# Performance work log

Hardware: AMD Instinct MI355X
Metric: run time of the kernel (lower is better)

Reference implementation:

```python
import jax, jax.numpy as jnp
import numpy as np
from jax import lax


def conv2d(x, w):
    # NCHW conv, stride 1, SAME padding, no bias (matches conv3x3/conv1x1 bias=False)
    return lax.conv_general_dilated(x, w, (1, 1), 'SAME',
                                    dimension_numbers=('NCHW', 'OIHW', 'NCHW'))


def scan_dir(x, w, b, axis, reverse):
    # IRNN recurrence along `axis`: h[t] = relu(w*h[t-1] + b + x[t]), h[0] = x[0]
    # w, b: per-channel scalars [C] (grouped 1x1 conv)
    xs = jnp.moveaxis(x, axis, 0)  # [T, B, C, L]
    if reverse:
        xs = xs[::-1]
    wb = w[None, :, None]
    bb = b[None, :, None]

    def step(h, xt):
        h = jax.nn.relu(wb * h + bb + xt)
        return h, h

    _, ys = lax.scan(step, xs[0], xs[1:])
    out = jnp.concatenate([xs[:1], ys], axis=0)
    if reverse:
        out = out[::-1]
    return jnp.moveaxis(out, 0, axis)


def irnn(x, ws, bs):
    # ws/bs: [4, C], direction order = up, right, down, left
    up = scan_dir(x, ws[0], bs[0], 2, True)
    right = scan_dir(x, ws[1], bs[1], 3, False)
    down = scan_dir(x, ws[2], bs[2], 2, False)
    left = scan_dir(x, ws[3], bs[3], 3, True)
    return jnp.concatenate([up, right, down, left], axis=1)  # [B, 4C, H, W]


def setup_inputs() -> dict:
    key = jax.random.key(0)
    ks = jax.random.split(key, 10)
    B, C, H, W = 8, 32, 256, 256
    x = jax.random.normal(ks[0], (B, C, H, W), jnp.float32)
    conv_in_w = jax.random.normal(ks[1], (C, C, 3, 3), jnp.float32) * 0.05
    conv2_w = jax.random.normal(ks[2], (C, 4 * C, 3, 3), jnp.float32) * 0.05
    conv3_w = jax.random.normal(ks[3], (C, 4 * C, 3, 3), jnp.float32) * 0.05
    conv_out_w = jax.random.normal(ks[4], (1, C, 1, 1), jnp.float32) * 0.05
    # grouped 1x1 conv weights: small magnitude keeps the 255-step recurrence stable
    irnn1_w = jax.random.uniform(ks[5], (4, C), jnp.float32, -0.2, 0.2)
    irnn1_b = jax.random.uniform(ks[6], (4, C), jnp.float32, -0.1, 0.1)
    irnn2_w = jax.random.uniform(ks[7], (4, C), jnp.float32, -0.2, 0.2)
    irnn2_b = jax.random.uniform(ks[8], (4, C), jnp.float32, -0.1, 0.1)
    return {"x": x, "conv_in_w": conv_in_w, "conv2_w": conv2_w,
            "conv3_w": conv3_w, "conv_out_w": conv_out_w,
            "irnn1_w": irnn1_w, "irnn1_b": irnn1_b,
            "irnn2_w": irnn2_w, "irnn2_b": irnn2_b}


def reference(x, conv_in_w, conv2_w, conv3_w, conv_out_w,
              irnn1_w, irnn1_b, irnn2_w, irnn2_b):
    # NOTE: torch's attention branch uses non-in-place .mul() whose result is
    # discarded, so attention has no effect on the output; omitted here.
    out = conv2d(x, conv_in_w)                                 # [B, C, H, W]
    out = conv2d(irnn(out, irnn1_w, irnn1_b), conv2_w)         # [B, C, H, W]
    out = jax.nn.relu(conv2d(irnn(out, irnn2_w, irnn2_b), conv3_w))
    mask = jax.nn.sigmoid(conv2d(out, conv_out_w))             # [B, 1, H, W]
    return mask
```

## Files before the change

kernel.cpp:

```cpp
#include <hip/hip_runtime.h>
#include <hip/hip_bf16.h>
#include <math.h>

static constexpr int Bn = 8, Cn = 32, Hn = 256, Wn = 256;
static constexpr int HP = 258;
static constexpr size_t PLANE = (size_t)Hn * Wn;

typedef __attribute__((ext_vector_type(8))) short bf16x8;
typedef __attribute__((ext_vector_type(4))) float f32x4;
typedef __attribute__((ext_vector_type(4))) short s16x4;
typedef __attribute__((ext_vector_type(4))) int   i32x4;

__device__ inline short bf16bits(float v) {
    union { __hip_bfloat16 h; short s; } u; u.h = __float2bfloat16(v);
    return u.s;
}
__device__ inline float bits2f(short s) {
    union { unsigned int u; float f; } u; u.u = ((unsigned int)(unsigned short)s) << 16;
    return u.f;
}
__device__ inline void async16(const short* g, short* l) {
    __builtin_amdgcn_global_load_lds(
        (const __attribute__((address_space(1))) unsigned int*)g,
        (__attribute__((address_space(3))) unsigned int*)l, 16, 0, 0);
}

template <int CIN>
__global__ __launch_bounds__(256) void pack_w(const float* __restrict__ w,
                                              __hip_bfloat16* __restrict__ wp)
{
    int idx = blockIdx.x * 256 + threadIdx.x;
    int j = idx & 7, g = (idx >> 3) & 3, m = (idx >> 5) & 15, mt = (idx >> 9) & 1;
    int rest = idx >> 10;
    int s = rest % 9, cb = rest / 9;
    int co = mt * 16 + m;
    int ci = cb * 32 + g * 8 + j;
    float v = w[((size_t)(co * CIN + ci) * 3 + s / 3) * 3 + (s % 3)];
    wp[idx] = __float2bfloat16(v);
}

template <int C>
__global__ __launch_bounds__(256) void zero_border(short* __restrict__ p)
{
    constexpr int CH8 = C / 8;
    int idx = blockIdx.x * 256 + threadIdx.x;
    if (idx >= 8 * 1028 * CH8) return;
    int c8 = idx % CH8;
    int rest = idx / CH8;
    int pe = rest % 1028, b = rest / 1028;
    int y, x;
    if (pe < 258)      { y = 0;   x = pe; }
    else if (pe < 516) { y = 257; x = pe - 258; }
    else if (pe < 772) { y = pe - 516 + 1; x = 0; }
    else               { y = pe - 772 + 1; x = 257; }
    *(i32x4*)(p + ((size_t)(b * HP + y) * HP + x) * C + c8 * 8) = i32x4{};
}

__global__ __launch_bounds__(256) void x_to_nhwc(const float* __restrict__ in,
                                                 __hip_bfloat16* __restrict__ out)
{
    __shared__ unsigned int shU[32 * 17];
    unsigned short* sh16 = (unsigned short*)shU;
    int tid = threadIdx.x;
    int px0 = blockIdx.x * 32;
    int b = blockIdx.y;
    const float2* in2 = (const float2*)(in + ((size_t)b * 32) * PLANE + px0);
    for (int i = tid; i < 512; i += 256) {
        int ch = i >> 4, pxp = i & 15;
        float2 v = in2[(size_t)ch * (PLANE / 2) + pxp];
        unsigned int lo = (unsigned short)bf16bits(v.x);
        unsigned int hi = (unsigned short)bf16bits(v.y);
        shU[ch * 17 + pxp] = lo | (hi << 16);
    }
    __syncthreads();
    int yy = px0 >> 8, xx0 = px0 & 255;
    unsigned int* out32 = (unsigned int*)out
        + ((size_t)(b * HP + yy + 1) * HP + xx0 + 1) * 16;
    for (int i = tid; i < 512; i += 256) {
        int px = i >> 4, chp = i & 15;
        unsigned int v = (unsigned int)sh16[(2 * chp) * 34 + px]
                       | ((unsigned int)sh16[(2 * chp + 1) * 34 + px] << 16);
        out32[(size_t)px * 16 + chp] = v;
    }
}

template <int CIN, bool RELU, bool FUSE>
__global__ __launch_bounds__(256, 2) void conv_mfma(const __hip_bfloat16* __restrict__ in,
        const __hip_bfloat16* __restrict__ wp, __hip_bfloat16* __restrict__ outA,
        const float* __restrict__ wo, float* __restrict__ outF)
{
    constexpr int CB = CIN / 32;
    constexpr int SLAB = 10880;
    constexpr int WSL  = 9216;
    constexpr int BUF  = SLAB + WSL;
    __shared__ short sIn[2 * BUF];
    int tid = threadIdx.x;
    int lane = tid & 63, wave = tid >> 6;
    int m = lane & 15, g = lane >> 4;
    int x0 = blockIdx.x * 32, y0 = blockIdx.y * 8, b = blockIdx.z;

    const short* inS = (const short*)in;
    const short* wpS = (const short*)wp;
    f32x4 acc[2][2][2] = {};

    auto stage = [&](int buf, int cb) {
        short* dst = sIn + buf * BUF;
        #pragma unroll
        for (int r = 0; r < 6; ++r) {
            int i = r * 256 + tid;
            if (r < 5 || i < 1360) {
                int ci16 = i & 3, q = i >> 2;
                int xx = q % 34, yy = q / 34;
                const short* gp = inS
                    + ((size_t)(b * HP + y0 + yy) * HP + x0 + xx) * CIN
                    + cb * 32 + ci16 * 8;
                async16(gp, dst + (r * 256 + wave * 64) * 8);
            }
        }
        #pragma unroll
        for (int r = 0; r < 5; ++r) {
            int i = r * 256 + tid;
            if (r < 4 || i < 1152) {
                const short* gp = wpS + (size_t)cb * WSL + i * 8;
                async16(gp, dst + SLAB * 1 + (r * 256 + wave * 64) * 8);
            }
        }
    };

    stage(0, 0);
    for (int cb = 0; cb < CB; ++cb) {
        __syncthreads();
        if (cb + 1 < CB) stage((cb + 1) & 1, cb + 1);
        const short* sb = sIn + (cb & 1) * BUF;
        const short* sw = sb + SLAB;

        #pragma unroll
        for (int s = 0; s < 9; ++s) {
            int dy = s / 3 - 1, dx = s % 3 - 1;
            bf16x8 wf0 = *(const bf16x8*)(sw + s * 1024 + (m * 4 + g) * 8);
            bf16x8 wf1 = *(const bf16x8*)(sw + s * 1024 + 512 + (m * 4 + g) * 8);
            #pragma unroll
            for (int wy = 0; wy < 2; ++wy) {
                int yy = wave * 2 + wy + dy + 1;
                const short* rp = sb + (yy * 34 + m + dx + 1) * 32 + g * 8;
                bf16x8 b0 = *(const bf16x8*)rp;
                bf16x8 b1 = *(const bf16x8*)(rp + 512);
                acc[wy][0][0] = __builtin_amdgcn_mfma_f32_16x16x32_bf16(wf0, b0, acc[wy][0][0], 0, 0, 0);
                acc[wy][1][0] = __builtin_amdgcn_mfma_f32_16x16x32_bf16(wf1, b0, acc[wy][1][0], 0, 0, 0);
                acc[wy][0][1] = __builtin_amdgcn_mfma_f32_16x16x32_bf16(wf0, b1, acc[wy][0][1], 0, 0, 0);
                acc[wy][1][1] = __builtin_amdgcn_mfma_f32_16x16x32_bf16(wf1, b1, acc[wy][1][1], 0, 0, 0);
            }
        }
    }

    if (FUSE) {
        float wv[2][4];
        #pragma unroll
        for (int mt = 0; mt < 2; ++mt)
            #pragma unroll
            for (int r = 0; r < 4; ++r) wv[mt][r] = wo[mt * 16 + g * 4 + r];
        #pragma unroll
        for (int wy = 0; wy < 2; ++wy) {
            int y = y0 + wave * 2 + wy;
            #pragma unroll
            for (int nt = 0; nt < 2; ++nt) {
                float s = 0.f;
                #pragma unroll
                for (int mt = 0; mt < 2; ++mt)
                    #pragma unroll
                    for (int r = 0; r < 4; ++r)
                        s = fmaf(fmaxf(acc[wy][mt][nt][r], 0.f), wv[mt][r], s);
                s += __shfl_xor(s, 16);
                s += __shfl_xor(s, 32);
                if (g == 0)
                    outF[(size_t)(b * 256 + y) * 256 + x0 + nt * 16 + m]
                        = 1.f / (1.f + expf(-s));
            }
        }
    } else {
        short* outS = (short*)outA;
        #pragma unroll
        for (int wy = 0; wy < 2; ++wy) {
            int y = y0 + wave * 2 + wy;
            #pragma unroll
            for (int nt = 0; nt < 2; ++nt) {
                int x = x0 + nt * 16 + m;
                size_t base = ((size_t)((b * 256 + y) * 256 + x)) * 32;
                #pragma unroll
                for (int mt = 0; mt < 2; ++mt) {
                    int co = mt * 16 + g * 4;
                    s16x4 ov;
                    #pragma unroll
                    for (int r = 0; r < 4; ++r) {
                        float v = acc[wy][mt][nt][r];
                        if (RELU) v = fmaxf(v, 0.f);
                        ov[r] = bf16bits(v);
                    }
                    *(s16x4*)(outS + base + co) = ov;
                }
            }
        }
    }
}

__global__ __launch_bounds__(256) void irnn_vert(const __hip_bfloat16* __restrict__ A,
        const float* __restrict__ w4, const float* __restrict__ b4,
        __hip_bfloat16* __restrict__ I)
{
    __shared__ short sA[64 * 256];
    int tid = threadIdx.x;
    int c = tid & 31, xo = tid >> 5;
    int x = blockIdx.x * 8 + xo;
    int y1 = blockIdx.y * 32;
    int b = blockIdx.z;
    const short* aS = (const short*)A;

    for (int i = tid; i < 2048; i += 256) {
        int slot = i >> 5, c8 = i & 31;
        int y = y1 - 16 + slot;
        if ((unsigned)y < (unsigned)Hn) {
            const short* gp = aS + ((size_t)(b * 256 + y) * 256 + blockIdx.x * 8) * 32 + c8 * 8;
            *(i32x4*)(sA + slot * 256 + c8 * 8) = *(const i32x4*)gp;
        }
    }
    __syncthreads();

    float wd = w4[2 * 32 + c], bd = b4[2 * 32 + c];
    float wu = w4[0 * 32 + c], bu = b4[0 * 32 + c];
    short* od = (short*)I + ((size_t)(b * HP + 1) * HP + 1 + x) * 128 + 2 * 32 + c;
    short* ou = (short*)I + ((size_t)(b * HP + 1) * HP + 1 + x) * 128 + 0 * 32 + c;
    const size_t os = (size_t)HP * 128;

    {
        int ys = y1 ? y1 - 16 : 0;
        float h = bits2f(sA[(ys - y1 + 16) * 256 + tid]);
        if (ys == y1) od[(size_t)y1 * os] = bf16bits(h);
        #pragma unroll 8
        for (int y = ys + 1; y < y1 + 32; ++y) {
            float xv = bits2f(sA[(y - y1 + 16) * 256 + tid]);
            h = fmaxf(fmaf(wd, h, bd + xv), 0.f);
            if (y >= y1) od[(size_t)y * os] = bf16bits(h);
        }
    }
    {
        int ye = (y1 + 47 > 255) ? 255 : y1 + 47;
        float h = bits2f(sA[(ye - y1 + 16) * 256 + tid]);
        if (ye == y1 + 31) ou[(size_t)ye * os] = bf16bits(h);
        #pragma unroll 8
        for (int y = ye - 1; y >= y1; --y) {
            float xv = bits2f(sA[(y - y1 + 16) * 256 + tid]);
            h = fmaxf(fmaf(wu, h, bu + xv), 0.f);
            if (y <= y1 + 31) ou[(size_t)y * os] = bf16bits(h);
        }
    }
}

__global__ __launch_bounds__(256) void irnn_horiz(const __hip_bfloat16* __restrict__ A,
        const float* __restrict__ w4, const float* __restrict__ b4,
        __hip_bfloat16* __restrict__ I)
{
    __shared__ short sA[8 * 64 * 32];
    int tid = threadIdx.x;
    int c = tid & 31, yo = tid >> 5;
    int y = blockIdx.x * 8 + yo;
    int x1 = blockIdx.y * 32;
    int b = blockIdx.z;
    const short* aS = (const short*)A;

    for (int i = tid; i < 2048; i += 256) {
        int yy = i >> 8, rem = i & 255;
        int slot = rem >> 2, c16 = rem & 3;
        int x = x1 - 16 + slot;
        if ((unsigned)x < (unsigned)Wn) {
            const short* gp = aS + ((size_t)(b * 256 + blockIdx.x * 8 + yy) * 256 + x) * 32 + c16 * 8;
            *(i32x4*)(sA + (yy * 64 + slot) * 32 + c16 * 8) = *(const i32x4*)gp;
        }
    }
    __syncthreads();

    float wr = w4[1 * 32 + c], br = b4[1 * 32 + c];
    float wl = w4[3 * 32 + c], bl = b4[3 * 32 + c];
    short* orr = (short*)I + ((size_t)(b * HP + 1 + y) * HP + 1) * 128 + 1 * 32 + c;
    short* ol  = (short*)I + ((size_t)(b * HP + 1 + y) * HP + 1) * 128 + 3 * 32 + c;
    const short* sRow = sA + yo * 64 * 32 + c;

    {
        int xs = x1 ? x1 - 16 : 0;
        float h = bits2f(sRow[(xs - x1 + 16) * 32]);
        if (xs == x1) orr[(size_t)x1 * 128] = bf16bits(h);
        #pragma unroll 8
        for (int x = xs + 1; x < x1 + 32; ++x) {
            float xv = bits2f(sRow[(x - x1 + 16) * 32]);
            h = fmaxf(fmaf(wr, h, br + xv), 0.f);
            if (x >= x1) orr[(size_t)x * 128] = bf16bits(h);
        }
    }
    {
        int xe = (x1 + 47 > 255) ? 255 : x1 + 47;
        float h = bits2f(sRow[(xe - x1 + 16) * 32]);
        if (xe == x1 + 31) ol[(size_t)xe * 128] = bf16bits(h);
        #pragma unroll 8
        for (int x = xe - 1; x >= x1; --x) {
            float xv = bits2f(sRow[(x - x1 + 16) * 32]);
            h = fmaxf(fmaf(wl, h, bl + xv), 0.f);
            if (x <= x1 + 31) ol[(size_t)x * 128] = bf16bits(h);
        }
    }
}

extern "C" void kernel_launch(void* const* d_in, const int* in_sizes, int n_in,
                              void* d_out, int out_size, void* d_ws, size_t ws_size,
                              hipStream_t stream)
{
    const float* x    = (const float*)d_in[0];
    const float* w_in = (const float*)d_in[1];
    const float* w2   = (const float*)d_in[2];
    const float* w3   = (const float*)d_in[3];
    const float* wo   = (const float*)d_in[4];
    const float* i1w  = (const float*)d_in[5];
    const float* i1b  = (const float*)d_in[6];
    const float* i2w  = (const float*)d_in[7];
    const float* i2b  = (const float*)d_in[8];
    float* out = (float*)d_out;

    char* ws = (char*)d_ws;
    __hip_bfloat16* Ipad  = (__hip_bfloat16*)ws;
    __hip_bfloat16* xTpad = (__hip_bfloat16*)ws;
    __hip_bfloat16* A = (__hip_bfloat16*)(ws + ((size_t)137 << 20));
    __hip_bfloat16* wp1 = (__hip_bfloat16*)(ws + ((size_t)170 << 20));
    __hip_bfloat16* wp2 = (__hip_bfloat16*)(ws + ((size_t)170 << 20) + ((size_t)1 << 19));
    __hip_bfloat16* wp3 = (__hip_bfloat16*)(ws + ((size_t)170 << 20) + ((size_t)2 << 19));

    dim3 convGrid(8, 32, 8);
    dim3 irnnGrid(32, 8, 8);

    pack_w<32> <<<36,  256, 0, stream>>>(w_in, wp1);
    pack_w<128><<<144, 256, 0, stream>>>(w2, wp2);
    pack_w<128><<<144, 256, 0, stream>>>(w3, wp3);

    zero_border<32><<<129, 256, 0, stream>>>((short*)xTpad);
    x_to_nhwc<<<dim3(2048, 8), 256, 0, stream>>>(x, xTpad);
    conv_mfma<32, false, false><<<convGrid, 256, 0, stream>>>(xTpad, wp1, A, nullptr, nullptr);

    zero_border<128><<<514, 256, 0, stream>>>((short*)Ipad);
    irnn_vert <<<irnnGrid, 256, 0, stream>>>(A, i1w, i1b, Ipad);
    irnn_horiz<<<irnnGrid, 256, 0, stream>>>(A, i1w, i1b, Ipad);
    conv_mfma<128, false, false><<<convGrid, 256, 0, stream>>>(Ipad, wp2, A, nullptr, nullptr);

    irnn_vert <<<irnnGrid, 256, 0, stream>>>(A, i2w, i2b, Ipad);
    irnn_horiz<<<irnnGrid, 256, 0, stream>>>(A, i2w, i2b, Ipad);
    conv_mfma<128, true, true><<<convGrid, 256, 0, stream>>>(Ipad, wp3, nullptr, wo, out);
}
```

Baseline: 314.3 us.

## Swizzle conv LDS layout, reuse B fragments across dy, drop LDS in IRNN scans

New measurement: 380.5 us. 1.21x slower.

```diff
diff --git a/kernel.cpp b/kernel.cpp
--- a/kernel.cpp
+++ b/kernel.cpp
@@ -19,6 +19,10 @@
     union { unsigned int u; float f; } u; u.u = ((unsigned int)(unsigned short)s) << 16;
     return u.f;
 }
+__device__ inline unsigned int pack2(float lo, float hi) {
+    return (unsigned int)(unsigned short)bf16bits(lo)
+         | ((unsigned int)(unsigned short)bf16bits(hi) << 16);
+}
 __device__ inline void async16(const short* g, short* l) {
     __builtin_amdgcn_global_load_lds(
         (const __attribute__((address_space(1))) unsigned int*)g,
@@ -30,9 +34,10 @@
                                               __hip_bfloat16* __restrict__ wp)
 {
     int idx = blockIdx.x * 256 + threadIdx.x;
-    int j = idx & 7, g = (idx >> 3) & 3, m = (idx >> 5) & 15, mt = (idx >> 9) & 1;
+    int j = idx & 7, gpos = (idx >> 3) & 3, m = (idx >> 5) & 15, mt = (idx >> 9) & 1;
     int rest = idx >> 10;
     int s = rest % 9, cb = rest / 9;
+    int g = gpos ^ ((m >> 2) & 3);
     int co = mt * 16 + m;
     int ci = cb * 32 + g * 8 + j;
     float v = w[((size_t)(co * CIN + ci) * 3 + s / 3) * 3 + (s % 3)];
@@ -109,11 +114,12 @@
         for (int r = 0; r < 6; ++r) {
             int i = r * 256 + tid;
             if (r < 5 || i < 1360) {
-                int ci16 = i & 3, q = i >> 2;
+                int gpos = i & 3, q = i >> 2;
                 int xx = q % 34, yy = q / 34;
+                int gl = gpos ^ ((xx >> 2) & 3);
                 const short* gp = inS
                     + ((size_t)(b * HP + y0 + yy) * HP + x0 + xx) * CIN
-                    + cb * 32 + ci16 * 8;
+                    + cb * 32 + gl * 8;
                 async16(gp, dst + (r * 256 + wave * 64) * 8);
             }
         }
@@ -122,10 +128,12 @@
             int i = r * 256 + tid;
             if (r < 4 || i < 1152) {
                 const short* gp = wpS + (size_t)cb * WSL + i * 8;
-                async16(gp, dst + SLAB * 1 + (r * 256 + wave * 64) * 8);
+                async16(gp, dst + SLAB + (r * 256 + wave * 64) * 8);
             }
         }
     };
+
+    int wfoff = (m * 4 + (g ^ ((m >> 2) & 3))) * 8;
 
     stage(0, 0);
     for (int cb = 0; cb < CB; ++cb) {
@@ -135,20 +143,29 @@
         const short* sw = sb + SLAB;
 
         #pragma unroll
-        for (int s = 0; s < 9; ++s) {
-            int dy = s / 3 - 1, dx = s % 3 - 1;
-            bf16x8 wf0 = *(const bf16x8*)(sw + s * 1024 + (m * 4 + g) * 8);
-            bf16x8 wf1 = *(const bf16x8*)(sw + s * 1024 + 512 + (m * 4 + g) * 8);
-            #pragma unroll
-            for (int wy = 0; wy < 2; ++wy) {
-                int yy = wave * 2 + wy + dy + 1;
-                const short* rp = sb + (yy * 34 + m + dx + 1) * 32 + g * 8;
-                bf16x8 b0 = *(const bf16x8*)rp;
-                bf16x8 b1 = *(const bf16x8*)(rp + 512);
-                acc[wy][0][0] = __builtin_amdgcn_mfma_f32_16x16x32_bf16(wf0, b0, acc[wy][0][0], 0, 0, 0);
-                acc[wy][1][0] = __builtin_amdgcn_mfma_f32_16x16x32_bf16(wf1, b0, acc[wy][1][0], 0, 0, 0);
-                acc[wy][0][1] = __builtin_amdgcn_mfma_f32_16x16x32_bf16(wf0, b1, acc[wy][0][1], 0, 0, 0);
-                acc[wy][1][1] = __builtin_amdgcn_mfma_f32_16x16x32_bf16(wf1, b1, acc[wy][1][1], 0, 0, 0);
+        for (int dxr = 0; dxr < 3; ++dxr) {
+            int xx = m + dxr;
+            const short* colp = sb + xx * 32 + (g ^ ((xx >> 2) & 3)) * 8;
+            bf16x8 Bf[4][2];
+            #pragma unroll
+            for (int rr = 0; rr < 4; ++rr) {
+                const short* rp = colp + (wave * 2 + rr) * (34 * 32);
+                Bf[rr][0] = *(const bf16x8*)rp;
+                Bf[rr][1] = *(const bf16x8*)(rp + 16 * 32);
+            }
+            #pragma unroll
+            for (int dyi = 0; dyi < 3; ++dyi) {
+                int s = dyi * 3 + dxr;
+                bf16x8 wf0 = *(const bf16x8*)(sw + s * 1024 + wfoff);
+                bf16x8 wf1 = *(const bf16x8*)(sw + s * 1024 + 512 + wfoff);
+                #pragma unroll
+                for (int wy = 0; wy < 2; ++wy) {
+                    int rr = wy + dyi;
+                    acc[wy][0][0] = __builtin_amdgcn_mfma_f32_16x16x32_bf16(wf0, Bf[rr][0], acc[wy][0][0], 0, 0, 0);
+                    acc[wy][1][0] = __builtin_amdgcn_mfma_f32_16x16x32_bf16(wf1, Bf[rr][0], acc[wy][1][0], 0, 0, 0);
+                    acc[wy][0][1] = __builtin_amdgcn_mfma_f32_16x16x32_bf16(wf0, Bf[rr][1], acc[wy][0][1], 0, 0, 0);
+                    acc[wy][1][1] = __builtin_amdgcn_mfma_f32_16x16x32_bf16(wf1, Bf[rr][1], acc[wy][1][1], 0, 0, 0);
+                }
             }
         }
     }
@@ -207,50 +224,45 @@
         const float* __restrict__ w4, const float* __restrict__ b4,
         __hip_bfloat16* __restrict__ I)
 {
-    __shared__ short sA[64 * 256];
     int tid = threadIdx.x;
-    int c = tid & 31, xo = tid >> 5;
-    int x = blockIdx.x * 8 + xo;
+    int c16 = tid & 15, xo = tid >> 4;
+    int x = blockIdx.x * 16 + xo;
     int y1 = blockIdx.y * 32;
     int b = blockIdx.z;
-    const short* aS = (const short*)A;
-
-    for (int i = tid; i < 2048; i += 256) {
-        int slot = i >> 5, c8 = i & 31;
-        int y = y1 - 16 + slot;
-        if ((unsigned)y < (unsigned)Hn) {
-            const short* gp = aS + ((size_t)(b * 256 + y) * 256 + blockIdx.x * 8) * 32 + c8 * 8;
-            *(i32x4*)(sA + slot * 256 + c8 * 8) = *(const i32x4*)gp;
-        }
-    }
-    __syncthreads();
-
-    float wd = w4[2 * 32 + c], bd = b4[2 * 32 + c];
-    float wu = w4[0 * 32 + c], bu = b4[0 * 32 + c];
-    short* od = (short*)I + ((size_t)(b * HP + 1) * HP + 1 + x) * 128 + 2 * 32 + c;
-    short* ou = (short*)I + ((size_t)(b * HP + 1) * HP + 1 + x) * 128 + 0 * 32 + c;
-    const size_t os = (size_t)HP * 128;
+    const unsigned int* ap = (const unsigned int*)A + ((size_t)b * PLANE + x) * 16 + c16;
+    unsigned int* ob = (unsigned int*)I + ((size_t)(b * HP + 1) * HP + 1 + x) * 64 + c16;
+    const size_t as = 256 * 16, os = (size_t)HP * 64;
 
     {
-        int ys = y1 ? y1 - 16 : 0;
-        float h = bits2f(sA[(ys - y1 + 16) * 256 + tid]);
-        if (ys == y1) od[(size_t)y1 * os] = bf16bits(h);
+        float w0 = w4[64 + 2 * c16], w1 = w4[64 + 2 * c16 + 1];
+        float B0 = b4[64 + 2 * c16], B1 = b4[64 + 2 * c16 + 1];
+        unsigned int* o = ob + 2 * 16;
+        int ys = y1 - 16; if (ys < 0) ys = 0;
+        unsigned int v = ap[(size_t)ys * as];
+        float h0 = bits2f((short)v), h1 = bits2f((short)(v >> 16));
+        if (ys == y1) o[(size_t)ys * os] = pack2(h0, h1);
         #pragma unroll 8
         for (int y = ys + 1; y < y1 + 32; ++y) {
-            float xv = bits2f(sA[(y - y1 + 16) * 256 + tid]);
-            h = fmaxf(fmaf(wd, h, bd + xv), 0.f);
-            if (y >= y1) od[(size_t)y * os] = bf16bits(h);
+            v = ap[(size_t)y * as];
+            h0 = fmaxf(fmaf(w0, h0, B0 + bits2f((short)v)), 0.f);
+            h1 = fmaxf(fmaf(w1, h1, B1 + bits2f((short)(v >> 16))), 0.f);
+            if (y >= y1) o[(size_t)y * os] = pack2(h0, h1);
         }
     }
     {
-        int ye = (y1 + 47 > 255) ? 255 : y1 + 47;
-        float h = bits2f(sA[(ye - y1 + 16) * 256 + tid]);
-        if (ye == y1 + 31) ou[(size_t)ye * os] = bf16bits(h);
+        float w0 = w4[2 * c16], w1 = w4[2 * c16 + 1];
+        float B0 = b4[2 * c16], B1 = b4[2 * c16 + 1];
+        unsigned int* o = ob;
+        int ye = y1 + 47; if (ye > 255) ye = 255;
+        unsigned int v = ap[(size_t)ye * as];
+        float h0 = bits2f((short)v), h1 = bits2f((short)(v >> 16));
+        if (ye == y1 + 31) o[(size_t)ye * os] = pack2(h0, h1);
         #pragma unroll 8
         for (int y = ye - 1; y >= y1; --y) {
-            float xv = bits2f(sA[(y - y1 + 16) * 256 + tid]);
-            h = fmaxf(fmaf(wu, h, bu + xv), 0.f);
-            if (y <= y1 + 31) ou[(size_t)y * os] = bf16bits(h);
+            v = ap[(size_t)y * as];
+            h0 = fmaxf(fmaf(w0, h0, B0 + bits2f((short)v)), 0.f);
+            h1 = fmaxf(fmaf(w1, h1, B1 + bits2f((short)(v >> 16))), 0.f);
+            if (y <= y1 + 31) o[(size_t)y * os] = pack2(h0, h1);
         }
     }
 }
@@ -259,51 +271,44 @@
         const float* __restrict__ w4, const float* __restrict__ b4,
         __hip_bfloat16* __restrict__ I)
 {
-    __shared__ short sA[8 * 64 * 32];
     int tid = threadIdx.x;
-    int c = tid & 31, yo = tid >> 5;
-    int y = blockIdx.x * 8 + yo;
+    int c16 = tid & 15, yo = tid >> 4;
+    int y = blockIdx.x * 16 + yo;
     int x1 = blockIdx.y * 32;
     int b = blockIdx.z;
-    const short* aS = (const short*)A;
-
-    for (int i = tid; i < 2048; i += 256) {
-        int yy = i >> 8, rem = i & 255;
-        int slot = rem >> 2, c16 = rem & 3;
-        int x = x1 - 16 + slot;
-        if ((unsigned)x < (unsigned)Wn) {
-            const short* gp = aS + ((size_t)(b * 256 + blockIdx.x * 8 + yy) * 256 + x) * 32 + c16 * 8;
-            *(i32x4*)(sA + (yy * 64 + slot) * 32 + c16 * 8) = *(const i32x4*)gp;
-        }
-    }
-    __syncthreads();
-
-    float wr = w4[1 * 32 + c], br = b4[1 * 32 + c];
-    float wl = w4[3 * 32 + c], bl = b4[3 * 32 + c];
-    short* orr = (short*)I + ((size_t)(b * HP + 1 + y) * HP + 1) * 128 + 1 * 32 + c;
-    short* ol  = (short*)I + ((size_t)(b * HP + 1 + y) * HP + 1) * 128 + 3 * 32 + c;
-    const short* sRow = sA + yo * 64 * 32 + c;
+    const unsigned int* ap = (const unsigned int*)A + ((size_t)b * PLANE + (size_t)y * 256) * 16 + c16;
+    unsigned int* ob = (unsigned int*)I + ((size_t)(b * HP + 1 + y) * HP + 1) * 64 + c16;
 
     {
-        int xs = x1 ? x1 - 16 : 0;
-        float h = bits2f(sRow[(xs - x1 + 16) * 32]);
-        if (xs == x1) orr[(size_t)x1 * 128] = bf16bits(h);
+        float w0 = w4[32 + 2 * c16], w1 = w4[32 + 2 * c16 + 1];
+        float B0 = b4[32 + 2 * c16], B1 = b4[32 + 2 * c16 + 1];
+        unsigned int* o = ob + 16;
+        int xs = x1 - 16; if (xs < 0) xs = 0;
+        unsigned int v = ap[(size_t)xs * 16];
+        float h0 = bits2f((short)v), h1 = bits2f((short)(v >> 16));
+        if (xs == x1) o[(size_t)xs * 64] = pack2(h0, h1);
         #pragma unroll 8
         for (int x = xs + 1; x < x1 + 32; ++x) {
-            float xv = bits2f(sRow[(x - x1 + 16) * 32]);
-            h = fmaxf(fmaf(wr, h, br + xv), 0.f);
-            if (x >= x1) orr[(size_t)x * 128] = bf16bits(h);
+            v = ap[(size_t)x * 16];
+            h0 = fmaxf(fmaf(w0, h0, B0 + bits2f((short)v)), 0.f);
+            h1 = fmaxf(fmaf(w1, h1, B1 + bits2f((short)(v >> 16))), 0.f);
+            if (x >= x1) o[(size_t)x * 64] = pack2(h0, h1);
         }
     }
     {
-        int xe = (x1 + 47 > 255) ? 255 : x1 + 47;
-        float h = bits2f(sRow[(xe - x1 + 16) * 32]);
-        if (xe == x1 + 31) ol[(size_t)xe * 128] = bf16bits(h);
+        float w0 = w4[96 + 2 * c16], w1 = w4[96 + 2 * c16 + 1];
+        float B0 = b4[96 + 2 * c16], B1 = b4[96 + 2 * c16 + 1];
+        unsigned int* o = ob + 48;
+        int xe = x1 + 47; if (xe > 255) xe = 255;
+        unsigned int v = ap[(size_t)xe * 16];
+        float h0 = bits2f((short)v), h1 = bits2f((short)(v >> 16));
+        if (xe == x1 + 31) o[(size_t)xe * 64] = pack2(h0, h1);
         #pragma unroll 8
         for (int x = xe - 1; x >= x1; --x) {
-            float xv = bits2f(sRow[(x - x1 + 16) * 32]);
-            h = fmaxf(fmaf(wl, h, bl + xv), 0.f);
-            if (x <= x1 + 31) ol[(size_t)x * 128] = bf16bits(h);
+            v = ap[(size_t)x * 16];
+            h0 = fmaxf(fmaf(w0, h0, B0 + bits2f((short)v)), 0.f);
+            h1 = fmaxf(fmaf(w1, h1, B1 + bits2f((short)(v >> 16))), 0.f);
+            if (x <= x1 + 31) o[(size_t)x * 64] = pack2(h0, h1);
         }
     }
 }
@@ -332,7 +337,7 @@
     __hip_bfloat16* wp3 = (__hip_bfloat16*)(ws + ((size_t)170 << 20) + ((size_t)2 << 19));
 
     dim3 convGrid(8, 32, 8);
-    dim3 irnnGrid(32, 8, 8);
+    dim3 irnnGrid(16, 8, 8);
 
     pack_w<32> <<<36,  256, 0, stream>>>(w_in, wp1);
     pack_w<128><<<144, 256, 0, stream>>>(w2, wp2);
```

## Use channel-blocked padded layout, XOR-swizzled LDS, and reuse B fragments across dy

Applied to the files above, without the earlier changes.

Result: no change. 309.9 us (-1.4%).

```diff
diff --git a/kernel.cpp b/kernel.cpp
--- a/kernel.cpp
+++ b/kernel.cpp
@@ -5,6 +5,7 @@
 static constexpr int Bn = 8, Cn = 32, Hn = 256, Wn = 256;
 static constexpr int HP = 258;
 static constexpr size_t PLANE = (size_t)Hn * Wn;
+static constexpr size_t PB = (size_t)HP * HP;
 
 typedef __attribute__((ext_vector_type(8))) short bf16x8;
 typedef __attribute__((ext_vector_type(4))) float f32x4;
@@ -30,30 +31,30 @@
                                               __hip_bfloat16* __restrict__ wp)
 {
     int idx = blockIdx.x * 256 + threadIdx.x;
-    int j = idx & 7, g = (idx >> 3) & 3, m = (idx >> 5) & 15, mt = (idx >> 9) & 1;
+    int j = idx & 7, gpos = (idx >> 3) & 3, m = (idx >> 5) & 15, mt = (idx >> 9) & 1;
     int rest = idx >> 10;
     int s = rest % 9, cb = rest / 9;
+    int g = gpos ^ ((m >> 2) & 3);
     int co = mt * 16 + m;
     int ci = cb * 32 + g * 8 + j;
     float v = w[((size_t)(co * CIN + ci) * 3 + s / 3) * 3 + (s % 3)];
     wp[idx] = __float2bfloat16(v);
 }
 
-template <int C>
+template <int NB>
 __global__ __launch_bounds__(256) void zero_border(short* __restrict__ p)
 {
-    constexpr int CH8 = C / 8;
     int idx = blockIdx.x * 256 + threadIdx.x;
-    if (idx >= 8 * 1028 * CH8) return;
-    int c8 = idx % CH8;
-    int rest = idx / CH8;
-    int pe = rest % 1028, b = rest / 1028;
+    if (idx >= NB * 1028 * 4) return;
+    int c8 = idx & 3;
+    int rest = idx >> 2;
+    int pe = rest % 1028, bb = rest / 1028;
     int y, x;
     if (pe < 258)      { y = 0;   x = pe; }
     else if (pe < 516) { y = 257; x = pe - 258; }
     else if (pe < 772) { y = pe - 516 + 1; x = 0; }
     else               { y = pe - 772 + 1; x = 257; }
-    *(i32x4*)(p + ((size_t)(b * HP + y) * HP + x) * C + c8 * 8) = i32x4{};
+    *(i32x4*)(p + ((size_t)bb * PB + (size_t)y * HP + x) * 32 + c8 * 8) = i32x4{};
 }
 
 __global__ __launch_bounds__(256) void x_to_nhwc(const float* __restrict__ in,
@@ -75,7 +76,7 @@
     __syncthreads();
     int yy = px0 >> 8, xx0 = px0 & 255;
     unsigned int* out32 = (unsigned int*)out
-        + ((size_t)(b * HP + yy + 1) * HP + xx0 + 1) * 16;
+        + ((size_t)b * PB + (size_t)(yy + 1) * HP + xx0 + 1) * 16;
     for (int i = tid; i < 512; i += 256) {
         int px = i >> 4, chp = i & 15;
         unsigned int v = (unsigned int)sh16[(2 * chp) * 34 + px]
@@ -109,11 +110,12 @@
         for (int r = 0; r < 6; ++r) {
             int i = r * 256 + tid;
             if (r < 5 || i < 1360) {
-                int ci16 = i & 3, q = i >> 2;
+                int gpos = i & 3, q = i >> 2;
                 int xx = q % 34, yy = q / 34;
+                int gl = gpos ^ ((xx >> 2) & 3);
                 const short* gp = inS
-                    + ((size_t)(b * HP + y0 + yy) * HP + x0 + xx) * CIN
-                    + cb * 32 + ci16 * 8;
+                    + ((size_t)(cb * 8 + b) * PB + (size_t)(y0 + yy) * HP + x0 + xx) * 32
+                    + gl * 8;
                 async16(gp, dst + (r * 256 + wave * 64) * 8);
             }
         }
@@ -122,10 +124,12 @@
             int i = r * 256 + tid;
             if (r < 4 || i < 1152) {
                 const short* gp = wpS + (size_t)cb * WSL + i * 8;
-                async16(gp, dst + SLAB * 1 + (r * 256 + wave * 64) * 8);
+                async16(gp, dst + SLAB + (r * 256 + wave * 64) * 8);
             }
         }
     };
+
+    int wfoff = (m * 4 + (g ^ ((m >> 2) & 3))) * 8;
 
     stage(0, 0);
     for (int cb = 0; cb < CB; ++cb) {
@@ -135,20 +139,29 @@
         const short* sw = sb + SLAB;
 
         #pragma unroll
-        for (int s = 0; s < 9; ++s) {
-            int dy = s / 3 - 1, dx = s % 3 - 1;
-            bf16x8 wf0 = *(const bf16x8*)(sw + s * 1024 + (m * 4 + g) * 8);
-            bf16x8 wf1 = *(const bf16x8*)(sw + s * 1024 + 512 + (m * 4 + g) * 8);
-            #pragma unroll
-            for (int wy = 0; wy < 2; ++wy) {
-                int yy = wave * 2 + wy + dy + 1;
-                const short* rp = sb + (yy * 34 + m + dx + 1) * 32 + g * 8;
-                bf16x8 b0 = *(const bf16x8*)rp;
-                bf16x8 b1 = *(const bf16x8*)(rp + 512);
-                acc[wy][0][0] = __builtin_amdgcn_mfma_f32_16x16x32_bf16(wf0, b0, acc[wy][0][0], 0, 0, 0);
-                acc[wy][1][0] = __builtin_amdgcn_mfma_f32_16x16x32_bf16(wf1, b0, acc[wy][1][0], 0, 0, 0);
-                acc[wy][0][1] = __builtin_amdgcn_mfma_f32_16x16x32_bf16(wf0, b1, acc[wy][0][1], 0, 0, 0);
-                acc[wy][1][1] = __builtin_amdgcn_mfma_f32_16x16x32_bf16(wf1, b1, acc[wy][1][1], 0, 0, 0);
+        for (int dxr = 0; dxr < 3; ++dxr) {
+            int xx = m + dxr;
+            const short* colp = sb + xx * 32 + (g ^ ((xx >> 2) & 3)) * 8;
+            bf16x8 Bf[4][2];
+            #pragma unroll
+            for (int rr = 0; rr < 4; ++rr) {
+                const short* rp = colp + (wave * 2 + rr) * (34 * 32);
+                Bf[rr][0] = *(const bf16x8*)rp;
+                Bf[rr][1] = *(const bf16x8*)(rp + 16 * 32);
+            }
+            #pragma unroll
+            for (int dyi = 0; dyi < 3; ++dyi) {
+                int s = dyi * 3 + dxr;
+                bf16x8 wf0 = *(const bf16x8*)(sw + s * 1024 + wfoff);
+                bf16x8 wf1 = *(const bf16x8*)(sw + s * 1024 + 512 + wfoff);
+                #pragma unroll
+                for (int wy = 0; wy < 2; ++wy) {
+                    int rr = wy + dyi;
+                    acc[wy][0][0] = __builtin_amdgcn_mfma_f32_16x16x32_bf16(wf0, Bf[rr][0], acc[wy][0][0], 0, 0, 0);
+                    acc[wy][1][0] = __builtin_amdgcn_mfma_f32_16x16x32_bf16(wf1, Bf[rr][0], acc[wy][1][0], 0, 0, 0);
+                    acc[wy][0][1] = __builtin_amdgcn_mfma_f32_16x16x32_bf16(wf0, Bf[rr][1], acc[wy][0][1], 0, 0, 0);
+                    acc[wy][1][1] = __builtin_amdgcn_mfma_f32_16x16x32_bf16(wf1, Bf[rr][1], acc[wy][1][1], 0, 0, 0);
+                }
             }
         }
     }
@@ -225,11 +238,11 @@
     }
     __syncthreads();
 
-    float wd = w4[2 * 32 + c], bd = b4[2 * 32 + c];
-    float wu = w4[0 * 32 + c], bu = b4[0 * 32 + c];
-    short* od = (short*)I + ((size_t)(b * HP + 1) * HP + 1 + x) * 128 + 2 * 32 + c;
-    short* ou = (short*)I + ((size_t)(b * HP + 1) * HP + 1 + x) * 128 + 0 * 32 + c;
-    const size_t os = (size_t)HP * 128;
+    float wd = w4[64 + c], bd = b4[64 + c];
+    float wu = w4[c],      bu = b4[c];
+    short* od = (short*)I + ((size_t)(2 * 8 + b) * PB + (size_t)HP + 1 + x) * 32 + c;
+    short* ou = (short*)I + ((size_t)(0 * 8 + b) * PB + (size_t)HP + 1 + x) * 32 + c;
+    const size_t os = (size_t)HP * 32;
 
     {
         int ys = y1 ? y1 - 16 : 0;
@@ -278,32 +291,32 @@
     }
     __syncthreads();
 
-    float wr = w4[1 * 32 + c], br = b4[1 * 32 + c];
-    float wl = w4[3 * 32 + c], bl = b4[3 * 32 + c];
-    short* orr = (short*)I + ((size_t)(b * HP + 1 + y) * HP + 1) * 128 + 1 * 32 + c;
-    short* ol  = (short*)I + ((size_t)(b * HP + 1 + y) * HP + 1) * 128 + 3 * 32 + c;
+    float wr = w4[32 + c], br = b4[32 + c];
+    float wl = w4[96 + c], bl = b4[96 + c];
+    short* orr = (short*)I + ((size_t)(1 * 8 + b) * PB + (size_t)(1 + y) * HP + 1) * 32 + c;
+    short* ol  = (short*)I + ((size_t)(3 * 8 + b) * PB + (size_t)(1 + y) * HP + 1) * 32 + c;
     const short* sRow = sA + yo * 64 * 32 + c;
 
     {
         int xs = x1 ? x1 - 16 : 0;
         float h = bits2f(sRow[(xs - x1 + 16) * 32]);
-        if (xs == x1) orr[(size_t)x1 * 128] = bf16bits(h);
+        if (xs == x1) orr[(size_t)x1 * 32] = bf16bits(h);
         #pragma unroll 8
         for (int x = xs + 1; x < x1 + 32; ++x) {
             float xv = bits2f(sRow[(x - x1 + 16) * 32]);
             h = fmaxf(fmaf(wr, h, br + xv), 0.f);
-            if (x >= x1) orr[(size_t)x * 128] = bf16bits(h);
+            if (x >= x1) orr[(size_t)x * 32] = bf16bits(h);
         }
     }
     {
         int xe = (x1 + 47 > 255) ? 255 : x1 + 47;
         float h = bits2f(sRow[(xe - x1 + 16) * 32]);
-        if (xe == x1 + 31) ol[(size_t)xe * 128] = bf16bits(h);
+        if (xe == x1 + 31) ol[(size_t)xe * 32] = bf16bits(h);
         #pragma unroll 8
         for (int x = xe - 1; x >= x1; --x) {
             float xv = bits2f(sRow[(x - x1 + 16) * 32]);
             h = fmaxf(fmaf(wl, h, bl + xv), 0.f);
-            if (x <= x1 + 31) ol[(size_t)x * 128] = bf16bits(h);
+            if (x <= x1 + 31) ol[(size_t)x * 32] = bf16bits(h);
         }
     }
 }
@@ -338,11 +351,10 @@
     pack_w<128><<<144, 256, 0, stream>>>(w2, wp2);
     pack_w<128><<<144, 256, 0, stream>>>(w3, wp3);
 
-    zero_border<32><<<129, 256, 0, stream>>>((short*)xTpad);
+    zero_border<32><<<514, 256, 0, stream>>>((short*)Ipad);
     x_to_nhwc<<<dim3(2048, 8), 256, 0, stream>>>(x, xTpad);
     conv_mfma<32, false, false><<<convGrid, 256, 0, stream>>>(xTpad, wp1, A, nullptr, nullptr);
 
-    zero_border<128><<<514, 256, 0, stream>>>((short*)Ipad);
     irnn_vert <<<irnnGrid, 256, 0, stream>>>(A, i1w, i1b, Ipad);
     irnn_horiz<<<irnnGrid, 256, 0, stream>>>(A, i1w, i1b, Ipad);
     conv_mfma<128, false, false><<<convGrid, 256, 0, stream>>>(Ipad, wp2, A, nullptr, nullptr);
```
